# Performance work log

Hardware: AMD Instinct MI355X
Metric: run time of the kernel (lower is better)

The kernel has to match this reference:

```python
import jax, jax.numpy as jnp
import numpy as np

D_MODEL = 2048
N_HEADS = 16
D_K = D_MODEL // N_HEADS
MAX_SEQ_LEN = 2048


def _rotary_tables(dim, max_seq_len):
    angular_freq = (1.0 / 10000.0) ** jnp.linspace(0.0, 1.0, dim // 2, dtype=jnp.float32)
    t = jnp.arange(max_seq_len, dtype=jnp.float32)
    theta = jnp.einsum('i,j->ij', t, angular_freq)  # [S, dk/2]
    return jnp.cos(theta), jnp.sin(theta)


def _apply_rotary(x, cos, sin):
    # x: [B, H, S, dk]; cos/sin: [S, dk/2]
    seq_len = x.shape[-2]
    c = cos[:seq_len][None, None]
    s = sin[:seq_len][None, None]
    x1, x2 = jnp.split(x, 2, axis=-1)
    y1 = x1 * c - x2 * s
    y2 = x1 * s + x2 * c
    return jnp.concatenate([y1, y2], axis=-1).astype(x.dtype)


def setup_inputs() -> dict:
    key = jax.random.key(0)
    k_x, k_qkv, k_o = jax.random.split(key, 3)
    B, S = 2, 2048
    x = jax.random.normal(k_x, (B, S, D_MODEL), dtype=jnp.float32)
    scale = 1.0 / np.sqrt(D_MODEL)
    w_qkv = jax.random.normal(k_qkv, (3 * D_MODEL, D_MODEL), dtype=jnp.float32) * scale
    w_o = jax.random.normal(k_o, (D_MODEL, D_MODEL), dtype=jnp.float32) * scale
    return {"x": x, "w_qkv": w_qkv, "w_o": w_o}


def reference(x, w_qkv, w_o):
    B, S, _ = x.shape
    cos, sin = _rotary_tables(D_K, MAX_SEQ_LEN)
    qkv = jnp.einsum('bsd,ed->bse', x, w_qkv)  # [B, S, 3*d_model]
    qkv = qkv.reshape(B, S, 3, N_HEADS, D_K).transpose(2, 0, 3, 1, 4)  # [3,B,H,S,dk]
    Q, K, V = qkv[0], qkv[1], qkv[2]
    Q = _apply_rotary(Q, cos, sin)
    K = _apply_rotary(K, cos, sin)
    scale = 1.0 / np.sqrt(D_K)
    scores = jnp.einsum('bhqd,bhkd->bhqk', Q, K) * scale
    causal = jnp.tril(jnp.ones((S, S), dtype=bool))
    scores = jnp.where(causal[None, None], scores, jnp.finfo(scores.dtype).min)
    attn = jax.nn.softmax(scores, axis=-1)
    out = jnp.einsum('bhqk,bhkd->bhqd', attn, V)  # [B,H,S,dk]
    out = out.transpose(0, 2, 1, 3).reshape(B, S, D_MODEL)
    return jnp.einsum('bsd,ed->bse', out, w_o)
```

## Files before the change

kernel.cpp:

```cpp
#include <hip/hip_runtime.h>
#include <hip/hip_bf16.h>


typedef __bf16 bf16;
typedef __bf16 bf16x4 __attribute__((ext_vector_type(4)));
typedef __bf16 bf16x8 __attribute__((ext_vector_type(8)));
typedef float f32x4 __attribute__((ext_vector_type(4)));
typedef float f32x16 __attribute__((ext_vector_type(16)));
typedef int i32x4 __attribute__((ext_vector_type(4)));

#define DEV __device__ __forceinline__

DEV void gll16(const void* g, void* lds_base_wave_uniform) {
  __builtin_amdgcn_global_load_lds((const __attribute__((address_space(1))) void*)g,
                                   (__attribute__((address_space(3))) void*)lds_base_wave_uniform,
                                   16, 0, 0);
}

DEV f32x4 mfma16(bf16x8 a, bf16x8 b, f32x4 c) {
  return __builtin_amdgcn_mfma_f32_16x16x32_bf16(a, b, c, 0, 0, 0);
}
DEV f32x16 mfma32(bf16x8 a, bf16x8 b, f32x16 c) {
  return __builtin_amdgcn_mfma_f32_32x32x16_bf16(a, b, c, 0, 0, 0);
}

DEV int cvtpk(float lo, float hi) {
  int r;
  asm("v_cvt_pk_bf16_f32 %0, %1, %2" : "=v"(r) : "v"(lo), "v"(hi));
  return r;
}

__global__ __launch_bounds__(256) void prep_all(const float* __restrict__ x,
                                                const float* __restrict__ wqkv,
                                                const float* __restrict__ wo,
                                                bf16* __restrict__ xb,
                                                bf16* __restrict__ wqkvb,
                                                bf16* __restrict__ wob,
                                                float* __restrict__ ctab,
                                                float* __restrict__ stab) {
  const int b = blockIdx.x;
  if (b < 12288) {
    const float* in;
    bf16* out;
    int bb = b;
    if (b < 4096) {
      in = x; out = xb;
    } else if (b < 10240) {
      in = wqkv; out = wqkvb; bb -= 4096;
    } else {
      in = wo; out = wob; bb -= 10240;
    }
    const int i = (bb * 256 + threadIdx.x) << 3;
    float4 a = *(const float4*)(in + i);
    float4 c = *(const float4*)(in + i + 4);
    bf16x8 o;
    o[0] = (bf16)a.x; o[1] = (bf16)a.y; o[2] = (bf16)a.z; o[3] = (bf16)a.w;
    o[4] = (bf16)c.x; o[5] = (bf16)c.y; o[6] = (bf16)c.z; o[7] = (bf16)c.w;
    *(bf16x8*)(out + i) = o;
  } else {
    const int id = (b - 12288) * 256 + threadIdx.x;
    const int s = id >> 6, j = id & 63;
    float freq = powf(10000.0f, -(float)j / 63.0f);
    float th = (float)s * freq;
    ctab[id] = cosf(th);
    stab[id] = sinf(th);
  }
}

__global__ __launch_bounds__(256) void rope_apply(bf16* __restrict__ Qb, bf16* __restrict__ Kb,
                                                  const float* __restrict__ ctab,
                                                  const float* __restrict__ stab) {
  const float QSCALE = 0.08838834764831845f * 1.4426950408889634f;
  int id = blockIdx.x * 256 + threadIdx.x;
  const int half = 32 * 2048 * 8;
  bf16* P = (id < half) ? Qb : Kb;
  const float scale = (id < half) ? QSCALE : 1.0f;
  int t = (id < half) ? id : id - half;
  const int d0 = (t & 7) << 3;
  const int s = (t >> 3) & 2047;
  const int bh = t >> 14;
  bf16* p = P + (((size_t)bh * 2048 + s) << 7);
  bf16x8 x1 = *(bf16x8*)(p + d0);
  bf16x8 x2 = *(bf16x8*)(p + d0 + 64);
  float4 ca = *(const float4*)(ctab + (s << 6) + d0);
  float4 cb = *(const float4*)(ctab + (s << 6) + d0 + 4);
  float4 sa = *(const float4*)(stab + (s << 6) + d0);
  float4 sb = *(const float4*)(stab + (s << 6) + d0 + 4);
  const float c[8] = {ca.x, ca.y, ca.z, ca.w, cb.x, cb.y, cb.z, cb.w};
  const float sn[8] = {sa.x, sa.y, sa.z, sa.w, sb.x, sb.y, sb.z, sb.w};
  bf16x8 y1, y2;
#pragma unroll
  for (int j = 0; j < 8; ++j) {
    const float a = (float)x1[j], b = (float)x2[j];
    y1[j] = (bf16)((a * c[j] - b * sn[j]) * scale);
    y2[j] = (bf16)((a * sn[j] + b * c[j]) * scale);
  }
  *(bf16x8*)(p + d0) = y1;
  *(bf16x8*)(p + d0 + 64) = y2;
}

__global__ __launch_bounds__(512, 2) void gemm384(const bf16* __restrict__ A,
                                                  const bf16* __restrict__ Bt,
                                                  bf16* __restrict__ q_out,
                                                  bf16* __restrict__ k_out,
                                                  bf16* __restrict__ v_out) {
  constexpr int K = 2048, NKT = 64;
  constexpr int BUFB = 40960;
  __shared__ char lds[3 * BUFB];
  const int id = blockIdx.x;
  const int swz = (id & 7) * 32 + (id >> 3);
  const int bx = swz & 15, by = swz >> 4;
  const int m0 = by << 8;
  const int n0 = bx * 384;
  const int tid = threadIdx.x, w = tid >> 6, l = tid & 63;
  const int wm = w >> 2, wn = w & 3;
  const int lsl = (l & 7) ^ ((l >> 3) & 7);
  const int srow = ((l >> 3) << 1) + (lsl >> 2);
  const int scol = (lsl & 3) << 3;

  auto STAGE = [&](int t, char* base) {
    const int k0 = t << 5;
#pragma unroll
    for (int c = 0; c < 2; ++c) {
      const int row = (c << 7) + (w << 4) + srow;
      gll16(A + (size_t)(m0 + row) * K + k0 + scol, base + (c << 13) + (w << 10));
    }
#pragma unroll
    for (int c = 0; c < 3; ++c) {
      const int row = (c << 7) + (w << 4) + srow;
      gll16(Bt + (size_t)(n0 + row) * K + k0 + scol, base + 16384 + (c << 13) + (w << 10));
    }
  };

  f32x4 acc[8][6] = {};

  STAGE(0, (char*)lds);
  STAGE(1, (char*)lds + BUFB);
  asm volatile("s_waitcnt vmcnt(5)" ::: "memory");
  __builtin_amdgcn_s_barrier();

#pragma unroll 1
  for (int t = 0, bi = 0, bj = 2; t < NKT; ++t) {
    char* rbase = (char*)lds + bi * BUFB;
    bf16x8 bfr[6];
#pragma unroll
    for (int j = 0; j < 6; ++j) {
      const int row = wn * 96 + (j << 4) + (l & 15);
      const int sr = row >> 1;
      bfr[j] = *(const bf16x8*)(rbase + 16384 + sr * 128 +
                                (((((row & 1) << 2) | (l >> 4)) ^ (sr & 7)) << 4));
    }
    bf16x8 af[4];
#pragma unroll
    for (int i = 0; i < 4; ++i) {
      const int row = (wm << 7) + (i << 4) + (l & 15);
      const int sr = row >> 1;
      af[i] = *(const bf16x8*)(rbase + sr * 128 +
                               (((((row & 1) << 2) | (l >> 4)) ^ (sr & 7)) << 4));
    }
    if (t + 2 < NKT) STAGE(t + 2, (char*)lds + bj * BUFB);
    asm volatile("s_waitcnt lgkmcnt(0)" ::: "memory");
    __builtin_amdgcn_sched_barrier(0);
    __builtin_amdgcn_s_setprio(1);
#pragma unroll
    for (int i = 0; i < 4; ++i)
#pragma unroll
      for (int j = 0; j < 6; ++j)
        acc[i][j] = mfma16(af[i], bfr[j], acc[i][j]);
    __builtin_amdgcn_s_setprio(0);
#pragma unroll
    for (int i = 0; i < 4; ++i) {
      const int row = (wm << 7) + 64 + (i << 4) + (l & 15);
      const int sr = row >> 1;
      af[i] = *(const bf16x8*)(rbase + sr * 128 +
                               (((((row & 1) << 2) | (l >> 4)) ^ (sr & 7)) << 4));
    }
    asm volatile("s_waitcnt lgkmcnt(0)" ::: "memory");
    __builtin_amdgcn_sched_barrier(0);
    __builtin_amdgcn_s_setprio(1);
#pragma unroll
    for (int i = 0; i < 4; ++i)
#pragma unroll
      for (int j = 0; j < 6; ++j)
        acc[4 + i][j] = mfma16(af[i], bfr[j], acc[4 + i][j]);
    __builtin_amdgcn_s_setprio(0);
    if (t + 2 < NKT) {
      asm volatile("s_waitcnt vmcnt(5)" ::: "memory");
    } else if (t + 2 == NKT) {
      asm volatile("s_waitcnt vmcnt(0)" ::: "memory");
    }
    __builtin_amdgcn_sched_barrier(0);
    __builtin_amdgcn_s_barrier();
    bi = (bi == 2) ? 0 : bi + 1;
    bj = (bj == 2) ? 0 : bj + 1;
  }

#pragma unroll
  for (int i = 0; i < 8; ++i)
#pragma unroll
    for (int j = 0; j < 6; ++j) {
      const int nl = n0 + wn * 96 + (j << 4) + (l & 15);
      const int which = nl >> 11;
      const int h = (nl >> 7) & 15, d = nl & 127;
      if (which < 2) {
        bf16* dst = which ? k_out : q_out;
#pragma unroll
        for (int r = 0; r < 4; ++r) {
          const int m = m0 + (wm << 7) + (i << 4) + ((l >> 4) << 2) + r;
          const int b_ = m >> 11, s = m & 2047;
          dst[(((size_t)((b_ << 4) | h)) * 2048 + s) * 128 + d] = (bf16)acc[i][j][r];
        }
      } else {
        const int sb = m0 + (wm << 7) + (i << 4) + ((l >> 4) << 2);
        const int b_ = sb >> 11, s = sb & 2047;
        bf16x4 vv;
#pragma unroll
        for (int r = 0; r < 4; ++r) vv[r] = (bf16)acc[i][j][r];
        *(bf16x4*)(v_out + ((size_t)((b_ << 4) | h) << 18) + ((size_t)d << 11) + s) = vv;
      }
    }
}

template <int NTN>
__global__ __launch_bounds__(256, 2) void gemm_o(const bf16* __restrict__ A,
                                                 const bf16* __restrict__ Bt,
                                                 float* __restrict__ f_out) {
  constexpr int K = 2048, NKT = 64;
  constexpr int BUFB = 16384;
  __shared__ char lds[3 * BUFB];
  const int nwg = 32 * NTN;
  const int id = blockIdx.x;
  const int swz = (id & 7) * (nwg >> 3) + (id >> 3);
  const int bx = swz % NTN, by = swz / NTN;
  const int m0 = by << 7, n0 = bx << 7;
  const int tid = threadIdx.x, w = tid >> 6, l = tid & 63;
  const int wm = w >> 1, wn = w & 1;
  const int lsl = (l & 7) ^ ((l >> 3) & 7);
  const int srow = ((l >> 3) << 1) + (lsl >> 2);
  const int scol = (lsl & 3) << 3;

  auto STAGE = [&](int t, char* base) {
    const int k0 = t << 5;
#pragma unroll
    for (int c = 0; c < 2; ++c) {
      const int row = (c << 6) + (w << 4) + srow;
      gll16(A + (size_t)(m0 + row) * K + k0 + scol, base + (c << 12) + (w << 10));
      gll16(Bt + (size_t)(n0 + row) * K + k0 + scol, base + 8192 + (c << 12) + (w << 10));
    }
  };

  f32x4 acc[4][4] = {};

  STAGE(0, (char*)lds);
  STAGE(1, (char*)lds + BUFB);
  asm volatile("s_waitcnt vmcnt(4)" ::: "memory");
  __builtin_amdgcn_s_barrier();

#pragma unroll 1
  for (int t = 0, bi = 0, bj = 2; t < NKT; ++t) {
    char* rbase = (char*)lds + bi * BUFB;
    bf16x8 af[4], bfr[4];
#pragma unroll
    for (int i = 0; i < 4; ++i) {
      const int row = (wm << 6) + (i << 4) + (l & 15);
      const int sr = row >> 1;
      af[i] = *(const bf16x8*)(rbase + sr * 128 +
                               (((((row & 1) << 2) | (l >> 4)) ^ (sr & 7)) << 4));
    }
#pragma unroll
    for (int j = 0; j < 4; ++j) {
      const int row = (wn << 6) + (j << 4) + (l & 15);
      const int sr = row >> 1;
      bfr[j] = *(const bf16x8*)(rbase + 8192 + sr * 128 +
                                (((((row & 1) << 2) | (l >> 4)) ^ (sr & 7)) << 4));
    }
    if (t + 2 < NKT) STAGE(t + 2, (char*)lds + bj * BUFB);
    asm volatile("s_waitcnt lgkmcnt(0)" ::: "memory");
    __builtin_amdgcn_sched_barrier(0);
    __builtin_amdgcn_s_setprio(1);
#pragma unroll
    for (int i = 0; i < 4; ++i)
#pragma unroll
      for (int j = 0; j < 4; ++j)
        acc[i][j] = mfma16(af[i], bfr[j], acc[i][j]);
    __builtin_amdgcn_s_setprio(0);
    if (t + 2 < NKT) {
      asm volatile("s_waitcnt vmcnt(4)" ::: "memory");
    } else if (t + 2 == NKT) {
      asm volatile("s_waitcnt vmcnt(0)" ::: "memory");
    }
    __builtin_amdgcn_sched_barrier(0);
    __builtin_amdgcn_s_barrier();
    bi = (bi == 2) ? 0 : bi + 1;
    bj = (bj == 2) ? 0 : bj + 1;
  }

#pragma unroll
  for (int i = 0; i < 4; ++i)
#pragma unroll
    for (int j = 0; j < 4; ++j)
#pragma unroll
      for (int r = 0; r < 4; ++r) {
        const int m = m0 + (wm << 6) + (i << 4) + ((l >> 4) << 2) + r;
        const int n = n0 + (wn << 6) + (j << 4) + (l & 15);
        f_out[(size_t)m * 2048 + n] = acc[i][j][r];
      }
}

__global__ __launch_bounds__(256, 2) void attn_kernel(const bf16* __restrict__ Qb,
                                                      const bf16* __restrict__ Kb,
                                                      const bf16* __restrict__ Vt,
                                                      bf16* __restrict__ Ao) {
  constexpr int S = 2048;
  __shared__ bf16 Ks[2][64 * 128];
  __shared__ bf16 Vs[2][128 * 64];
  const int id = blockIdx.x;
  const int swz = (id & 7) * 64 + (id >> 3);
  const int bh = swz >> 4;
  int qt = swz & 15;
  if ((swz >> 5) & 1) qt = 15 - qt;
  const int q0 = qt << 7;
  const int tid = threadIdx.x, w = tid >> 6, l = tid & 63;
  const int hi = l >> 5;
  const bf16* Qp = Qb + ((size_t)bh << 18);
  const bf16* Kp = Kb + ((size_t)bh << 18);
  const bf16* Vp = Vt + ((size_t)bh << 18);

  auto STAGE_KV = [&](int kv0, int bufi) {
    char* Kbase = (char*)Ks + (bufi << 14);
    char* Vbase = (char*)Vs + (bufi << 14);
#pragma unroll
    for (int i = 0; i < 4; ++i) {
      const int rk = (w << 4) + (i << 2) + (l >> 4);
      gll16(Kp + ((size_t)(kv0 + rk) << 7) + (((l & 15) ^ (rk & 7)) << 3),
            Kbase + (w << 12) + (i << 10));
      const int rv = (w << 5) + (i << 3) + (l >> 3);
      gll16(Vp + (size_t)rv * S + kv0 + (((l & 7) ^ (rv & 7)) << 3),
            Vbase + (w << 12) + (i << 10));
    }
  };

  bf16x8 qf[8];
#pragma unroll
  for (int kt = 0; kt < 8; ++kt)
    qf[kt] = *(const bf16x8*)(Qp + ((size_t)(q0 + (w << 5) + (l & 31)) << 7) + (kt << 4) + (hi << 3));

  f32x16 o[4] = {};
  float mrun = -3e38f, lrun = 0.f;

  const int qminw = q0 + (w << 5);
  const int qmaxw = qminw + 31;
  const int kv_end = q0 + 128;

  STAGE_KV(0, 0);
  __syncthreads();

  int bufi = 0;
#pragma unroll 1
  for (int kv0 = 0; kv0 < kv_end; kv0 += 64, bufi ^= 1) {
    if (kv0 + 64 < kv_end) STAGE_KV(kv0 + 64, bufi ^ 1);
    if (kv0 <= qmaxw) {
      const char* Kbase = (const char*)Ks + (bufi << 14);
      const char* Vbase = (const char*)Vs + (bufi << 14);
      f32x16 sc0 = {}, sc1 = {};
      __builtin_amdgcn_s_setprio(1);
#pragma unroll
      for (int kt = 0; kt < 8; ++kt) {
        const int rk0 = l & 31;
        const int coff = ((kt << 5) + (hi << 4));
        bf16x8 k0 = *(const bf16x8*)(Kbase + (rk0 << 8) + (coff ^ ((rk0 & 7) << 4)));
        bf16x8 k1 = *(const bf16x8*)(Kbase + ((rk0 + 32) << 8) + (coff ^ ((rk0 & 7) << 4)));
        sc0 = mfma32(k0, qf[kt], sc0);
        sc1 = mfma32(k1, qf[kt], sc1);
      }
      __builtin_amdgcn_s_setprio(0);
      if (kv0 + 63 > qminw) {
        const int qg = qminw + (l & 31);
#pragma unroll
        for (int r = 0; r < 16; ++r) {
          const int kvr = kv0 + (r & 3) + ((r >> 2) << 3) + (hi << 2);
          if (kvr > qg) sc0[r] = -3e38f;
          if (kvr + 32 > qg) sc1[r] = -3e38f;
        }
      }
      float mx = -3e38f;
#pragma unroll
      for (int r = 0; r < 16; ++r) mx = fmaxf(mx, fmaxf(sc0[r], sc1[r]));
      mx = fmaxf(mx, __shfl_xor(mx, 32));
      const float mnew = fmaxf(mrun, mx);
      if (!__all(mx <= mrun)) {
        const float alpha = exp2f(mrun - mnew);
        lrun *= alpha;
#pragma unroll
        for (int dt = 0; dt < 4; ++dt) o[dt] *= alpha;
      }
      mrun = mnew;
      float ps = 0.f;
#pragma unroll
      for (int r = 0; r < 16; ++r) {
        sc0[r] = exp2f(sc0[r] - mnew); ps += sc0[r];
        sc1[r] = exp2f(sc1[r] - mnew); ps += sc1[r];
      }
      ps += __shfl_xor(ps, 32);
      lrun += ps;
#pragma unroll
      for (int ks = 0; ks < 4; ++ks) {
        const f32x16& s = (ks & 2) ? sc1 : sc0;
        const int rb = (ks & 1) << 3;
        int pa_ = cvtpk(s[rb + 0], s[rb + 1]);
        int pb_ = cvtpk(s[rb + 2], s[rb + 3]);
        int pc_ = cvtpk(s[rb + 4], s[rb + 5]);
        int pd_ = cvtpk(s[rb + 6], s[rb + 7]);
        int sa = __shfl_xor(pa_, 32), sb = __shfl_xor(pb_, 32);
        int sc_ = __shfl_xor(pc_, 32), sd = __shfl_xor(pd_, 32);
        i32x4 pi;
        pi[0] = hi ? sc_ : pa_;
        pi[1] = hi ? sd : pb_;
        pi[2] = hi ? pc_ : sa;
        pi[3] = hi ? pd_ : sb;
        const bf16x8 pf = __builtin_bit_cast(bf16x8, pi);
        __builtin_amdgcn_s_setprio(1);
#pragma unroll
        for (int dt = 0; dt < 4; ++dt) {
          const int rd = (dt << 5) + (l & 31);
          const bf16x8 vf = *(const bf16x8*)(Vbase + (rd << 7) +
                                             (((ks << 5) + (hi << 4)) ^ ((rd & 7) << 4)));
          o[dt] = mfma32(vf, pf, o[dt]);
        }
        __builtin_amdgcn_s_setprio(0);
      }
    }
    __syncthreads();
  }
  const float rinv = 1.0f / lrun;
  const int b = bh >> 4, h = bh & 15;
  const int qg = q0 + (w << 5) + (l & 31);
  bf16* Arow = Ao + (((size_t)(b * S + qg)) << 11) + (h << 7);
#pragma unroll
  for (int dt = 0; dt < 4; ++dt)
#pragma unroll
    for (int g = 0; g < 4; ++g) {
      bf16x4 ov;
#pragma unroll
      for (int r = 0; r < 4; ++r) ov[r] = (bf16)(o[dt][(g << 2) + r] * rinv);
      *(bf16x4*)(Arow + (dt << 5) + (g << 3) + (hi << 2)) = ov;
    }
}

extern "C" void kernel_launch(void* const* d_in, const int* in_sizes, int n_in,
                              void* d_out, int out_size, void* d_ws, size_t ws_size,
                              hipStream_t stream) {
  const float* x = (const float*)d_in[0];
  const float* w_qkv = (const float*)d_in[1];
  const float* w_o = (const float*)d_in[2];
  float* out = (float*)d_out;
  char* ws = (char*)d_ws;

  bf16* xb    = (bf16*)(ws);
  bf16* wqkvb = (bf16*)(ws + (16ull << 20));
  bf16* wob   = (bf16*)(ws + (40ull << 20));
  bf16* Qb    = (bf16*)(ws + (48ull << 20));
  bf16* Kb    = (bf16*)(ws + (64ull << 20));
  bf16* Vt    = (bf16*)(ws + (80ull << 20));
  bf16* Ao    = (bf16*)(ws + (96ull << 20));
  float* ctab = (float*)(ws + (112ull << 20));
  float* stab = (float*)(ws + (113ull << 20));

  prep_all<<<12800, 256, 0, stream>>>(x, w_qkv, w_o, xb, wqkvb, wob, ctab, stab);
  gemm384<<<256, 512, 0, stream>>>(xb, wqkvb, Qb, Kb, Vt);
  rope_apply<<<4096, 256, 0, stream>>>(Qb, Kb, ctab, stab);
  attn_kernel<<<512, 256, 0, stream>>>(Qb, Kb, Vt, Ao);
  gemm_o<16><<<512, 256, 0, stream>>>(Ao, wob, out);
}
```

Baseline: 250.0 us.

## Fuse RoPE into QKV GEMM epilogue for K and attention prologue for Q

Removes the standalone rope_apply kernel. The QKV GEMM remaps each wave's B-fragment columns so it holds both rotary halves (d and d+64) of a head, which lets it apply RoPE to K in the epilogue before storing. Q is still stored unrotated, and the attention kernel rotates and scales its Q fragments in registers after loading them. This saves one full read-modify-write pass over Q and K plus a kernel launch. In exchange it adds cos/sin table loads to the GEMM epilogue and the attention prologue, and may cost more registers.

```diff
diff --git a/kernel.cpp b/kernel.cpp
--- a/kernel.cpp
+++ b/kernel.cpp
@@ -67,43 +67,13 @@
   }
 }
 
-__global__ __launch_bounds__(256) void rope_apply(bf16* __restrict__ Qb, bf16* __restrict__ Kb,
-                                                  const float* __restrict__ ctab,
-                                                  const float* __restrict__ stab) {
-  const float QSCALE = 0.08838834764831845f * 1.4426950408889634f;
-  int id = blockIdx.x * 256 + threadIdx.x;
-  const int half = 32 * 2048 * 8;
-  bf16* P = (id < half) ? Qb : Kb;
-  const float scale = (id < half) ? QSCALE : 1.0f;
-  int t = (id < half) ? id : id - half;
-  const int d0 = (t & 7) << 3;
-  const int s = (t >> 3) & 2047;
-  const int bh = t >> 14;
-  bf16* p = P + (((size_t)bh * 2048 + s) << 7);
-  bf16x8 x1 = *(bf16x8*)(p + d0);
-  bf16x8 x2 = *(bf16x8*)(p + d0 + 64);
-  float4 ca = *(const float4*)(ctab + (s << 6) + d0);
-  float4 cb = *(const float4*)(ctab + (s << 6) + d0 + 4);
-  float4 sa = *(const float4*)(stab + (s << 6) + d0);
-  float4 sb = *(const float4*)(stab + (s << 6) + d0 + 4);
-  const float c[8] = {ca.x, ca.y, ca.z, ca.w, cb.x, cb.y, cb.z, cb.w};
-  const float sn[8] = {sa.x, sa.y, sa.z, sa.w, sb.x, sb.y, sb.z, sb.w};
-  bf16x8 y1, y2;
-#pragma unroll
-  for (int j = 0; j < 8; ++j) {
-    const float a = (float)x1[j], b = (float)x2[j];
-    y1[j] = (bf16)((a * c[j] - b * sn[j]) * scale);
-    y2[j] = (bf16)((a * sn[j] + b * c[j]) * scale);
-  }
-  *(bf16x8*)(p + d0) = y1;
-  *(bf16x8*)(p + d0 + 64) = y2;
-}
-
 __global__ __launch_bounds__(512, 2) void gemm384(const bf16* __restrict__ A,
                                                   const bf16* __restrict__ Bt,
                                                   bf16* __restrict__ q_out,
                                                   bf16* __restrict__ k_out,
-                                                  bf16* __restrict__ v_out) {
+                                                  bf16* __restrict__ v_out,
+                                                  const float* __restrict__ ctab,
+                                                  const float* __restrict__ stab) {
   constexpr int K = 2048, NKT = 64;
   constexpr int BUFB = 40960;
   __shared__ char lds[3 * BUFB];
@@ -145,7 +115,7 @@
     bf16x8 bfr[6];
 #pragma unroll
     for (int j = 0; j < 6; ++j) {
-      const int row = wn * 96 + (j << 4) + (l & 15);
+      const int row = ((j >> 1) << 7) + ((j & 1) << 6) + (wn << 4) + (l & 15);
       const int sr = row >> 1;
       bfr[j] = *(const bf16x8*)(rbase + 16384 + sr * 128 +
                                 (((((row & 1) << 2) | (l >> 4)) ^ (sr & 7)) << 4));
@@ -195,30 +165,52 @@
     bj = (bj == 2) ? 0 : bj + 1;
   }
 
-#pragma unroll
-  for (int i = 0; i < 8; ++i)
-#pragma unroll
-    for (int j = 0; j < 6; ++j) {
-      const int nl = n0 + wn * 96 + (j << 4) + (l & 15);
-      const int which = nl >> 11;
-      const int h = (nl >> 7) & 15, d = nl & 127;
-      if (which < 2) {
-        bf16* dst = which ? k_out : q_out;
+  const int d2 = (wn << 4) + (l & 15);
+#pragma unroll
+  for (int i = 0; i < 8; ++i) {
+    const int mbase = m0 + (wm << 7) + (i << 4) + ((l >> 4) << 2);
+    const int b_ = mbase >> 11, sbase = mbase & 2047;
+    float cc[4], ss[4];
+    if (((n0 + 256) >> 11) == 1 || (n0 >> 11) == 1) {
+#pragma unroll
+      for (int r = 0; r < 4; ++r) {
+        cc[r] = ctab[((sbase + r) << 6) + d2];
+        ss[r] = stab[((sbase + r) << 6) + d2];
+      }
+    }
+#pragma unroll
+    for (int p = 0; p < 3; ++p) {
+      const int nb = n0 + (p << 7);
+      const int which = nb >> 11;
+      const int h = (nb >> 7) & 15;
+      if (which == 0) {
+        const size_t base = (((size_t)((b_ << 4) | h)) * 2048 + sbase) * 128;
 #pragma unroll
         for (int r = 0; r < 4; ++r) {
-          const int m = m0 + (wm << 7) + (i << 4) + ((l >> 4) << 2) + r;
-          const int b_ = m >> 11, s = m & 2047;
-          dst[(((size_t)((b_ << 4) | h)) * 2048 + s) * 128 + d] = (bf16)acc[i][j][r];
+          q_out[base + ((size_t)r << 7) + d2]      = (bf16)acc[i][2 * p][r];
+          q_out[base + ((size_t)r << 7) + d2 + 64] = (bf16)acc[i][2 * p + 1][r];
+        }
+      } else if (which == 1) {
+        const size_t base = (((size_t)((b_ << 4) | h)) * 2048 + sbase) * 128;
+#pragma unroll
+        for (int r = 0; r < 4; ++r) {
+          const float x1 = acc[i][2 * p][r], x2 = acc[i][2 * p + 1][r];
+          k_out[base + ((size_t)r << 7) + d2]      = (bf16)(x1 * cc[r] - x2 * ss[r]);
+          k_out[base + ((size_t)r << 7) + d2 + 64] = (bf16)(x1 * ss[r] + x2 * cc[r]);
         }
       } else {
-        const int sb = m0 + (wm << 7) + (i << 4) + ((l >> 4) << 2);
-        const int b_ = sb >> 11, s = sb & 2047;
-        bf16x4 vv;
-#pragma unroll
-        for (int r = 0; r < 4; ++r) vv[r] = (bf16)acc[i][j][r];
-        *(bf16x4*)(v_out + ((size_t)((b_ << 4) | h) << 18) + ((size_t)d << 11) + s) = vv;
-      }
-    }
+        bf16x4 v1, v2;
+#pragma unroll
+        for (int r = 0; r < 4; ++r) {
+          v1[r] = (bf16)acc[i][2 * p][r];
+          v2[r] = (bf16)acc[i][2 * p + 1][r];
+        }
+        const size_t hb = ((size_t)((b_ << 4) | h) << 18);
+        *(bf16x4*)(v_out + hb + ((size_t)d2 << 11) + sbase) = v1;
+        *(bf16x4*)(v_out + hb + ((size_t)(d2 + 64) << 11) + sbase) = v2;
+      }
+    }
+  }
 }
 
 template <int NTN>
@@ -310,7 +302,9 @@
 __global__ __launch_bounds__(256, 2) void attn_kernel(const bf16* __restrict__ Qb,
                                                       const bf16* __restrict__ Kb,
                                                       const bf16* __restrict__ Vt,
-                                                      bf16* __restrict__ Ao) {
+                                                      bf16* __restrict__ Ao,
+                                                      const float* __restrict__ ctab,
+                                                      const float* __restrict__ stab) {
   constexpr int S = 2048;
   __shared__ bf16 Ks[2][64 * 128];
   __shared__ bf16 Vs[2][128 * 64];
@@ -340,10 +334,33 @@
     }
   };
 
+  STAGE_KV(0, 0);
+
+  const int sq = q0 + (w << 5) + (l & 31);
   bf16x8 qf[8];
 #pragma unroll
   for (int kt = 0; kt < 8; ++kt)
-    qf[kt] = *(const bf16x8*)(Qp + ((size_t)(q0 + (w << 5) + (l & 31)) << 7) + (kt << 4) + (hi << 3));
+    qf[kt] = *(const bf16x8*)(Qp + ((size_t)sq << 7) + (kt << 4) + (hi << 3));
+  {
+    const float QS = 0.08838834764831845f * 1.4426950408889634f;
+#pragma unroll
+    for (int kt = 0; kt < 4; ++kt) {
+      const int d2 = (kt << 4) + (hi << 3);
+      const float* cp = ctab + (sq << 6) + d2;
+      const float* sp = stab + (sq << 6) + d2;
+      float4 c0 = *(const float4*)cp, c1 = *(const float4*)(cp + 4);
+      float4 s0 = *(const float4*)sp, s1 = *(const float4*)(sp + 4);
+      const float cA[8] = {c0.x, c0.y, c0.z, c0.w, c1.x, c1.y, c1.z, c1.w};
+      const float sA[8] = {s0.x, s0.y, s0.z, s0.w, s1.x, s1.y, s1.z, s1.w};
+      const bf16x8 lo = qf[kt], up = qf[kt + 4];
+#pragma unroll
+      for (int j2 = 0; j2 < 8; ++j2) {
+        const float a = (float)lo[j2], b2 = (float)up[j2];
+        qf[kt][j2]     = (bf16)((a * cA[j2] - b2 * sA[j2]) * QS);
+        qf[kt + 4][j2] = (bf16)((a * sA[j2] + b2 * cA[j2]) * QS);
+      }
+    }
+  }
 
   f32x16 o[4] = {};
   float mrun = -3e38f, lrun = 0.f;
@@ -352,7 +369,6 @@
   const int qmaxw = qminw + 31;
   const int kv_end = q0 + 128;
 
-  STAGE_KV(0, 0);
   __syncthreads();
 
   int bufi = 0;
@@ -434,8 +450,7 @@
   }
   const float rinv = 1.0f / lrun;
   const int b = bh >> 4, h = bh & 15;
-  const int qg = q0 + (w << 5) + (l & 31);
-  bf16* Arow = Ao + (((size_t)(b * S + qg)) << 11) + (h << 7);
+  bf16* Arow = Ao + (((size_t)(b * S + sq)) << 11) + (h << 7);
 #pragma unroll
   for (int dt = 0; dt < 4; ++dt)
 #pragma unroll
@@ -467,8 +482,7 @@
   float* stab = (float*)(ws + (113ull << 20));
 
   prep_all<<<12800, 256, 0, stream>>>(x, w_qkv, w_o, xb, wqkvb, wob, ctab, stab);
-  gemm384<<<256, 512, 0, stream>>>(xb, wqkvb, Qb, Kb, Vt);
-  rope_apply<<<4096, 256, 0, stream>>>(Qb, Kb, ctab, stab);
-  attn_kernel<<<512, 256, 0, stream>>>(Qb, Kb, Vt, Ao);
+  gemm384<<<256, 512, 0, stream>>>(xb, wqkvb, Qb, Kb, Vt, ctab, stab);
+  attn_kernel<<<512, 256, 0, stream>>>(Qb, Kb, Vt, Ao, ctab, stab);
   gemm_o<16><<<512, 256, 0, stream>>>(Ao, wob, out);
 }
```

Result: faster. 244.9 us (-2.0%).
